# Optimization experiments

Measured on AMD Instinct MI355X. Metric: run time of the kernel, lower is better.

## Reference

```python
import jax, jax.numpy as jnp
import numpy as np


def setup_inputs() -> dict:
    key = jax.random.key(0)
    ks = jax.random.split(key, 8)
    b, n, K, d, MC = 32, 64, 512, 256, 2
    # soft codebook assignments per slot (bounded convex weights)
    encodings = jax.nn.softmax(jax.random.normal(ks[0], (b, n, K), jnp.float32), axis=-1)
    # hypersphere-initialized means (unit-norm rows)
    mu = jax.random.normal(ks[1], (K, d), jnp.float32)
    mu_embeddings = mu / jnp.linalg.norm(mu, axis=-1, keepdims=True)
    sigma_embeddings = jax.random.uniform(ks[2], (K, d), jnp.float32)
    fc1_w = jax.random.normal(ks[3], (K, d, d), jnp.float32) * (1.0 / np.sqrt(d))
    fc1_b = jax.random.normal(ks[4], (K, d), jnp.float32) * 0.02
    fc2_w = jax.random.normal(ks[5], (K, d, d), jnp.float32) * (1.0 / np.sqrt(d))
    fc2_b = jax.random.normal(ks[6], (K, d), jnp.float32) * 0.02
    eps = jax.random.normal(ks[7], (b, MC, n, d), jnp.float32)  # reparam noise
    return {"encodings": encodings, "mu_embeddings": mu_embeddings,
            "sigma_embeddings": sigma_embeddings, "fc1_w": fc1_w, "fc1_b": fc1_b,
            "fc2_w": fc2_w, "fc2_b": fc2_b, "eps": eps}


def reference(encodings, mu_embeddings, sigma_embeddings, fc1_w, fc1_b, fc2_w, fc2_b, eps):
    b, n, K = encodings.shape
    m = eps.shape[1]
    # per-slot Gaussian params from codebook mixture
    slot_mu = jnp.einsum('bnk,kd->bnd', encodings, mu_embeddings)          # (b,n,d)
    slot_sigma = jnp.exp(0.5 * jnp.einsum('bnk,kd->bnd', encodings, sigma_embeddings))
    # reparameterized MC samples: (b,m,n,d)
    slots = slot_mu[:, None] + slot_sigma[:, None] * eps
    # per-token dynamic 2-layer MLP weights (mixture over codebook)
    fc1w = jnp.einsum('bnk,kgh->bngh', encodings, fc1_w)  # (b,n,d,d)
    fc1b = jnp.einsum('bnk,kg->bng', encodings, fc1_b)    # (b,n,d)
    fc2w = jnp.einsum('bnk,kgh->bngh', encodings, fc2_w)
    fc2b = jnp.einsum('bnk,kg->bng', encodings, fc2_b)
    slots = jax.nn.relu(jnp.einsum('bmng,bngh->bmnh', slots, fc1w) + fc1b[:, None])
    slots = jax.nn.relu(jnp.einsum('bmng,bngh->bmnh', slots, fc2w) + fc2b[:, None])
    # rearrange 'b m n d -> (b m) n d'
    return slots.reshape(b * m, n, slots.shape[-1])
```

## Files before the change

### kernel.cpp

```cpp
#include <hip/hip_runtime.h>
#include <hip/hip_bf16.h>

typedef unsigned short u16;
typedef __attribute__((ext_vector_type(8))) short shortx8;
typedef __attribute__((ext_vector_type(4))) float floatx4;

__device__ __forceinline__ float bf2f(u16 u) {
    union { unsigned int ui; float f; } x; x.ui = ((unsigned int)u) << 16; return x.f;
}
__device__ __forceinline__ u16 f2b(float f) {
    union { float f; unsigned int u; } x; x.f = f;
    unsigned int r = (x.u + 0x7fffu + ((x.u >> 16) & 1u)) >> 16;
    return (u16)r;
}
__device__ __forceinline__ void glds16(const void* g, void* l) {
    __builtin_amdgcn_global_load_lds((const __attribute__((address_space(1))) void*)g,
                                     (__attribute__((address_space(3))) void*)l, 16, 0, 0);
}

__global__ __launch_bounds__(256) void cvt_bf16_kernel(const float* __restrict__ src,
                                                       u16* __restrict__ dst, int n) {
    int i = (blockIdx.x * 256 + threadIdx.x) * 4;
    if (i + 3 < n) {
        float4 v = *(const float4*)&src[i];
        ushort4 o; o.x = f2b(v.x); o.y = f2b(v.y); o.z = f2b(v.z); o.w = f2b(v.w);
        *(ushort4*)&dst[i] = o;
    }
}

__global__ __launch_bounds__(256) void build_bsmall_t(const float* __restrict__ mu,
                                                      const float* __restrict__ sg,
                                                      const float* __restrict__ b1,
                                                      const float* __restrict__ b2,
                                                      u16* __restrict__ Bs) {
    __shared__ float t[32][33];
    const float* src;
    int z = blockIdx.z;
    if (z == 0) src = mu; else if (z == 1) src = sg; else if (z == 2) src = b1; else src = b2;
    int k0 = blockIdx.x * 32, c0 = blockIdx.y * 32;
    int r = threadIdx.x >> 3, c4 = (threadIdx.x & 7) * 4;
    float4 v = *(const float4*)&src[(size_t)(k0 + r) * 256 + c0 + c4];
    t[r][c4] = v.x; t[r][c4 + 1] = v.y; t[r][c4 + 2] = v.z; t[r][c4 + 3] = v.w;
    __syncthreads();
    ushort4 o;
    o.x = f2b(t[c4 + 0][r]); o.y = f2b(t[c4 + 1][r]);
    o.z = f2b(t[c4 + 2][r]); o.w = f2b(t[c4 + 3][r]);
    *(ushort4*)&Bs[(size_t)(z * 256 + c0 + r) * 512 + k0 + c4] = o;
}

__global__ __launch_bounds__(256) void cvt_transpose(const float* __restrict__ W,
                                                     u16* __restrict__ Bt) {
    __shared__ float t[64][33];
    int n0 = blockIdx.x * 32, k0 = blockIdx.y * 64;
    int r = threadIdx.x >> 2;
    int c = (threadIdx.x & 3) * 8;
    float4 v0 = *(const float4*)&W[(size_t)(k0 + r) * 65536 + n0 + c];
    float4 v1 = *(const float4*)&W[(size_t)(k0 + r) * 65536 + n0 + c + 4];
    t[r][c + 0] = v0.x; t[r][c + 1] = v0.y; t[r][c + 2] = v0.z; t[r][c + 3] = v0.w;
    t[r][c + 4] = v1.x; t[r][c + 5] = v1.y; t[r][c + 6] = v1.z; t[r][c + 7] = v1.w;
    __syncthreads();
    int nr = threadIdx.x >> 3;
    int kk = (threadIdx.x & 7) * 8;
    shortx8 o;
    #pragma unroll
    for (int i = 0; i < 8; i++) o[i] = (short)f2b(t[kk + i][nr]);
    *(shortx8*)&Bt[(size_t)(n0 + nr) * 512 + k0 + kk] = o;
}

__global__ __launch_bounds__(256) void slots_kernel(const float* __restrict__ P,
                                                    const float* __restrict__ eps,
                                                    float* __restrict__ slots) {
    int t = blockIdx.x, d = threadIdx.x;
    float mu = P[(size_t)t * 1024 + d];
    float sg = expf(0.5f * P[(size_t)t * 1024 + 256 + d]);
    int b = t >> 6, n = t & 63;
    #pragma unroll
    for (int m = 0; m < 2; m++) {
        float e = eps[(size_t)(((b * 2 + m) * 64) + n) * 256 + d];
        slots[(size_t)t * 512 + m * 256 + d] = mu + sg * e;
    }
}

__global__ __launch_bounds__(256, 2) void gemm_small(const u16* __restrict__ A,
                                                     const u16* __restrict__ B,
                                                     float* __restrict__ C,
                                                     int N, int K,
                                                     int nbx_l2, int bypx_l2) {
    __shared__ __align__(16) u16 As[128 * 64];
    __shared__ __align__(16) u16 Bs[128 * 64];
    int tid = threadIdx.x;
    int wave = tid >> 6, lane = tid & 63;

    int id = blockIdx.x;
    int xcd = id & 7, sq = id >> 3;
    int by = (xcd << bypx_l2) + (sq >> nbx_l2);
    int bx = sq & ((1 << nbx_l2) - 1);
    int m0 = bx * 128, n0 = by * 128;
    int wm = wave >> 1, wn = wave & 1;

    floatx4 acc[4][4];
    #pragma unroll
    for (int r = 0; r < 4; r++)
        #pragma unroll
        for (int c = 0; c < 4; c++)
            #pragma unroll
            for (int q = 0; q < 4; q++) acc[r][c][q] = 0.f;

    int lrsub = lane >> 3, kcl = lane & 7;
    const u16* gA[4]; const u16* gB[4]; u16* lA[4]; u16* lB[4];
    #pragma unroll
    for (int j = 0; j < 4; j++) {
        int r0 = (wave * 4 + j) * 8;
        int row = r0 + lrsub;
        int kof = (kcl ^ (row & 7)) * 8;
        gA[j] = A + (size_t)(m0 + row) * K + kof;
        gB[j] = B + (size_t)(n0 + row) * K + kof;
        lA[j] = As + r0 * 64;
        lB[j] = Bs + r0 * 64;
    }

    int arb = wm * 64 + (lane & 15);
    int brb = wn * 64 + (lane & 15);
    int axr = arb & 7, bxr = brb & 7;
    int cl0 = lane >> 4;

    for (int k0 = 0; k0 < K; k0 += 64) {
        #pragma unroll
        for (int j = 0; j < 4; j++) glds16(gA[j] + k0, lA[j]);
        #pragma unroll
        for (int j = 0; j < 4; j++) glds16(gB[j] + k0, lB[j]);
        __syncthreads();
        #pragma unroll
        for (int s = 0; s < 2; s++) {
            shortx8 af[4], bf[4];
            int ac = ((s * 4 + cl0) ^ axr) * 8;
            int bc = ((s * 4 + cl0) ^ bxr) * 8;
            #pragma unroll
            for (int r = 0; r < 4; r++) af[r] = *(const shortx8*)(As + (arb + r * 16) * 64 + ac);
            #pragma unroll
            for (int c = 0; c < 4; c++) bf[c] = *(const shortx8*)(Bs + (brb + c * 16) * 64 + bc);
            #pragma unroll
            for (int r = 0; r < 4; r++)
                #pragma unroll
                for (int c = 0; c < 4; c++)
                    acc[r][c] = __builtin_amdgcn_mfma_f32_16x16x32_bf16(af[r], bf[c], acc[r][c], 0, 0, 0);
        }
        __syncthreads();
    }

    int crow0 = m0 + wm * 64 + (lane >> 4) * 4;
    int ccol  = n0 + wn * 64 + (lane & 15);
    #pragma unroll
    for (int r = 0; r < 4; r++)
        #pragma unroll
        for (int c = 0; c < 4; c++)
            #pragma unroll
            for (int q = 0; q < 4; q++)
                C[(size_t)(crow0 + r * 16 + q) * N + ccol + c * 16] = acc[r][c][q];
}

__global__ __launch_bounds__(256) void init_y(const float* __restrict__ P,
                                              float* __restrict__ Y, int bias_col) {
    int t = blockIdx.x, h = threadIdx.x;
    float b = P[(size_t)t * 1024 + bias_col + h];
    Y[((size_t)t * 2 + 0) * 256 + h] = b;
    Y[((size_t)t * 2 + 1) * 256 + h] = b;
}

__global__ __launch_bounds__(256, 2) void fused_mlp(const u16* __restrict__ Eb,
                                                    const u16* __restrict__ Bt,
                                                    const float* __restrict__ S,
                                                    float* __restrict__ Y,
                                                    int relu_s) {
    __shared__ __align__(16) u16 As[2][128 * 64];
    __shared__ __align__(16) u16 Bs[2][2][64 * 64];
    int tid = threadIdx.x;
    int wave = tid >> 6, lane = tid & 63;

    int id = blockIdx.x;
    int xcd = id & 7;
    int rest = id >> 3;
    int tt = rest & 15;
    int chi = rest >> 4;
    int combo = chi * 8 + xcd;
    int hh = combo >> 3;
    int gg = combo & 7;
    int m0 = tt * 128;
    int h0 = hh * 64;
    int g0 = gg * 32;

    int wm = wave >> 1, wn = wave & 1;
    int lrsub = lane >> 3, kcl = lane & 7;
    int kof = (kcl ^ lrsub) * 8;

    const u16* gAb = Eb + (size_t)(m0 + wave * 32 + lrsub) * 512 + kof;
    const u16* gBb = Bt + ((size_t)g0 * 256 + h0 + wave * 16 + lrsub) * 512 + kof;

    int arb = wm * 64 + (lane & 15);
    int brb = wn * 32 + (lane & 15);
    int axr = arb & 7, bxr = brb & 7;
    int cl0 = lane >> 4;

    floatx4 yreg[2][4][2];
    #pragma unroll
    for (int m = 0; m < 2; m++)
        #pragma unroll
        for (int r = 0; r < 4; r++)
            #pragma unroll
            for (int c = 0; c < 2; c++)
                #pragma unroll
                for (int q = 0; q < 4; q++) yreg[m][r][c][q] = 0.f;

    #pragma unroll
    for (int j = 0; j < 4; j++) glds16(gAb + j * 4096, &As[0][wave * 2048 + j * 512]);
    #pragma unroll
    for (int j = 0; j < 2; j++) glds16(gBb + j * 4096, &Bs[0][0][wave * 1024 + j * 512]);
    #pragma unroll
    for (int j = 0; j < 2; j++) glds16(gBb + 131072 + j * 4096, &Bs[0][1][wave * 1024 + j * 512]);

    const float* Sb = S + (size_t)(m0 + wm * 64 + cl0 * 4) * 512 + g0;

    #pragma unroll 1
    for (int gp = 0; gp < 16; gp++) {
        floatx4 acc[2][4][2];
        #pragma unroll
        for (int u = 0; u < 2; u++)
            #pragma unroll
            for (int r = 0; r < 4; r++)
                #pragma unroll
                for (int c = 0; c < 2; c++)
                    #pragma unroll
                    for (int q = 0; q < 4; q++) acc[u][r][c][q] = 0.f;

        #pragma unroll
        for (int ks = 0; ks < 8; ++ks) {
            const int cb = ks & 1;
            const int nb = cb ^ 1;
            {
                const int nk = ((ks + 1) & 7) * 64;
                const int ngp = (ks == 7) ? ((gp + 1) & 15) : gp;
                const size_t ng = (size_t)(2 * ngp) * 131072;
                #pragma unroll
                for (int j = 0; j < 4; j++)
                    glds16(gAb + j * 4096 + nk, &As[nb][wave * 2048 + j * 512]);
                #pragma unroll
                for (int j = 0; j < 2; j++)
                    glds16(gBb + ng + j * 4096 + nk, &Bs[nb][0][wave * 1024 + j * 512]);
                #pragma unroll
                for (int j = 0; j < 2; j++)
                    glds16(gBb + ng + 131072 + j * 4096 + nk, &Bs[nb][1][wave * 1024 + j * 512]);
            }
            asm volatile("s_waitcnt vmcnt(8)" ::: "memory");
            __builtin_amdgcn_s_barrier();
            __builtin_amdgcn_sched_barrier(0);
            #pragma unroll
            for (int s = 0; s < 2; s++) {
                shortx8 af[4], bf[2][2];
                int ac = ((s * 4 + cl0) ^ axr) * 8;
                int bc = ((s * 4 + cl0) ^ bxr) * 8;
                #pragma unroll
                for (int r = 0; r < 4; r++)
                    af[r] = *(const shortx8*)(&As[cb][(arb + r * 16) * 64 + ac]);
                #pragma unroll
                for (int u = 0; u < 2; u++)
                    #pragma unroll
                    for (int c = 0; c < 2; c++)
                        bf[u][c] = *(const shortx8*)(&Bs[cb][u][(brb + c * 16) * 64 + bc]);
                #pragma unroll
                for (int r = 0; r < 4; r++)
                    #pragma unroll
                    for (int u = 0; u < 2; u++)
                        #pragma unroll
                        for (int c = 0; c < 2; c++)
                            acc[u][r][c] = __builtin_amdgcn_mfma_f32_16x16x32_bf16(af[r], bf[u][c], acc[u][r][c], 0, 0, 0);
            }
            __builtin_amdgcn_sched_barrier(0);
            __builtin_amdgcn_s_barrier();
        }

        #pragma unroll
        for (int u = 0; u < 2; u++) {
            int gi = 2 * gp + u;
            #pragma unroll
            for (int m = 0; m < 2; m++)
                #pragma unroll
                for (int r = 0; r < 4; r++)
                    #pragma unroll
                    for (int q = 0; q < 4; q++) {
                        float sv = Sb[(size_t)(r * 16 + q) * 512 + m * 256 + gi];
                        if (relu_s) sv = fmaxf(sv, 0.f);
                        #pragma unroll
                        for (int c = 0; c < 2; c++)
                            yreg[m][r][c][q] += sv * acc[u][r][c][q];
                    }
        }
    }

    asm volatile("s_waitcnt vmcnt(0)" ::: "memory");

    int l16 = lane & 15;
    #pragma unroll
    for (int m = 0; m < 2; m++)
        #pragma unroll
        for (int r = 0; r < 4; r++)
            #pragma unroll
            for (int c = 0; c < 2; c++)
                #pragma unroll
                for (int q = 0; q < 4; q++) {
                    int t = m0 + wm * 64 + cl0 * 4 + r * 16 + q;
                    int h = h0 + wn * 32 + c * 16 + l16;
                    atomicAdd(&Y[((size_t)t * 2 + m) * 256 + h], yreg[m][r][c][q]);
                }
}

__global__ __launch_bounds__(256) void final_out(const float* __restrict__ Y,
                                                 float* __restrict__ out) {
    int t = blockIdx.x, h = threadIdx.x;
    int b = t >> 6, n = t & 63;
    #pragma unroll
    for (int m = 0; m < 2; m++)
        out[((size_t)((b * 2 + m) * 64) + n) * 256 + h] =
            fmaxf(Y[((size_t)t * 2 + m) * 256 + h], 0.f);
}

extern "C" void kernel_launch(void* const* d_in, const int* in_sizes, int n_in,
                              void* d_out, int out_size, void* d_ws, size_t ws_size,
                              hipStream_t stream) {
    const float* enc = (const float*)d_in[0];
    const float* mu  = (const float*)d_in[1];
    const float* sg  = (const float*)d_in[2];
    const float* f1w = (const float*)d_in[3];
    const float* f1b = (const float*)d_in[4];
    const float* f2w = (const float*)d_in[5];
    const float* f2b = (const float*)d_in[6];
    const float* eps = (const float*)d_in[7];
    float* out = (float*)d_out;

    size_t off = 0;
    auto alloc = [&](size_t b) -> char* {
        char* p = (char*)d_ws + off; off += (b + 255) & ~(size_t)255; return p;
    };
    u16*   Eb    = (u16*)  alloc((size_t)2048 * 512 * 2);
    float* P     = (float*)alloc((size_t)2048 * 1024 * 4);
    float* slots = (float*)alloc((size_t)2048 * 512 * 4);
    float* Y1    = (float*)alloc((size_t)2048 * 512 * 4);
    float* Y2    = (float*)alloc((size_t)2048 * 512 * 4);
    u16*   Bsm   = (u16*)  alloc((size_t)1024 * 512 * 2);
    u16*   Bt    = (u16*)  alloc((size_t)65536 * 512 * 2);

    cvt_bf16_kernel<<<1024, 256, 0, stream>>>(enc, Eb, 2048 * 512);
    build_bsmall_t<<<dim3(16, 8, 4), 256, 0, stream>>>(mu, sg, f1b, f2b, Bsm);
    gemm_small<<<128, 256, 0, stream>>>(Eb, Bsm, P, 1024, 512, 4, 0);
    slots_kernel<<<2048, 256, 0, stream>>>(P, eps, slots);

    cvt_transpose<<<dim3(2048, 8), 256, 0, stream>>>(f1w, Bt);
    init_y<<<2048, 256, 0, stream>>>(P, Y1, 512);
    fused_mlp<<<512, 256, 0, stream>>>(Eb, Bt, slots, Y1, 0);

    cvt_transpose<<<dim3(2048, 8), 256, 0, stream>>>(f2w, Bt);
    init_y<<<2048, 256, 0, stream>>>(P, Y2, 768);
    fused_mlp<<<512, 256, 0, stream>>>(Eb, Bt, Y1, Y2, 1);

    final_out<<<2048, 256, 0, stream>>>(Y2, out);
}
```

Measured before the change: 707.2 us.

## Stage slot activations in LDS, single-buffer A tiles, fold bias init into slots

The two init_y launches are merged into the slots kernel, which now also writes the broadcast fc biases into Y1 and Y2. In fused_mlp, the slot activations used for the per-g weighting (with the ReLU applied) are staged once into LDS in two halves, replacing strided global loads in the epilogue. To free LDS for this, the A tile drops from double to single buffering and is loaded at the current k-step rather than prefetched. That exposes A-load latency on every k-step, and a leftover dead loop adds a wasted global read.

Measured after the change: 721.3 us. No clear change (+2.0%).

```diff
diff --git a/kernel.cpp b/kernel.cpp
--- a/kernel.cpp
+++ b/kernel.cpp
@@ -67,12 +67,20 @@
     *(shortx8*)&Bt[(size_t)(n0 + nr) * 512 + k0 + kk] = o;
 }
 
-__global__ __launch_bounds__(256) void slots_kernel(const float* __restrict__ P,
-                                                    const float* __restrict__ eps,
-                                                    float* __restrict__ slots) {
+__global__ __launch_bounds__(256) void slots_init(const float* __restrict__ P,
+                                                  const float* __restrict__ eps,
+                                                  float* __restrict__ slots,
+                                                  float* __restrict__ Y1,
+                                                  float* __restrict__ Y2) {
     int t = blockIdx.x, d = threadIdx.x;
     float mu = P[(size_t)t * 1024 + d];
     float sg = expf(0.5f * P[(size_t)t * 1024 + 256 + d]);
+    float b1 = P[(size_t)t * 1024 + 512 + d];
+    float b2 = P[(size_t)t * 1024 + 768 + d];
+    Y1[((size_t)t * 2 + 0) * 256 + d] = b1;
+    Y1[((size_t)t * 2 + 1) * 256 + d] = b1;
+    Y2[((size_t)t * 2 + 0) * 256 + d] = b2;
+    Y2[((size_t)t * 2 + 1) * 256 + d] = b2;
     int b = t >> 6, n = t & 63;
     #pragma unroll
     for (int m = 0; m < 2; m++) {
@@ -159,21 +167,14 @@
                 C[(size_t)(crow0 + r * 16 + q) * N + ccol + c * 16] = acc[r][c][q];
 }
 
-__global__ __launch_bounds__(256) void init_y(const float* __restrict__ P,
-                                              float* __restrict__ Y, int bias_col) {
-    int t = blockIdx.x, h = threadIdx.x;
-    float b = P[(size_t)t * 1024 + bias_col + h];
-    Y[((size_t)t * 2 + 0) * 256 + h] = b;
-    Y[((size_t)t * 2 + 1) * 256 + h] = b;
-}
-
 __global__ __launch_bounds__(256, 2) void fused_mlp(const u16* __restrict__ Eb,
                                                     const u16* __restrict__ Bt,
                                                     const float* __restrict__ S,
                                                     float* __restrict__ Y,
                                                     int relu_s) {
-    __shared__ __align__(16) u16 As[2][128 * 64];
+    __shared__ __align__(16) u16 As[128 * 64];
     __shared__ __align__(16) u16 Bs[2][2][64 * 64];
+    __shared__ float sl[128 * 2 * 16];
     int tid = threadIdx.x;
     int wave = tid >> 6, lane = tid & 63;
 
@@ -189,6 +190,25 @@
     int h0 = hh * 64;
     int g0 = gg * 32;
 
+    {
+        int g = tid & 15, m = (tid >> 4) & 1, tb = tid >> 5;
+        for (int p = 0; p < 16; p++) {
+            int t = tb + p * 8;
+            float v = S[((size_t)(m0 + t) * 2 + m) * 256 + g0 + g];
+            if (relu_s) v = fmaxf(v, 0.f);
+            sl[(t * 2 + m) * 16 + g] = v;
+        }
+        int g2 = g + 16;
+        for (int p = 0; p < 16; p++) {
+            int t = tb + p * 8;
+            float v = S[((size_t)(m0 + t) * 2 + m) * 256 + g0 + g2];
+            if (relu_s) v = fmaxf(v, 0.f);
+            (void)v; (void)g2;
+            break;
+        }
+    }
+    __syncthreads();
+
     int wm = wave >> 1, wn = wave & 1;
     int lrsub = lane >> 3, kcl = lane & 7;
     int kof = (kcl ^ lrsub) * 8;
@@ -212,16 +232,23 @@
                 for (int q = 0; q < 4; q++) yreg[m][r][c][q] = 0.f;
 
     #pragma unroll
-    for (int j = 0; j < 4; j++) glds16(gAb + j * 4096, &As[0][wave * 2048 + j * 512]);
-    #pragma unroll
     for (int j = 0; j < 2; j++) glds16(gBb + j * 4096, &Bs[0][0][wave * 1024 + j * 512]);
     #pragma unroll
     for (int j = 0; j < 2; j++) glds16(gBb + 131072 + j * 4096, &Bs[0][1][wave * 1024 + j * 512]);
-
-    const float* Sb = S + (size_t)(m0 + wm * 64 + cl0 * 4) * 512 + g0;
 
     #pragma unroll 1
     for (int gp = 0; gp < 16; gp++) {
+        if (gp == 8) {
+            __syncthreads();
+            int g = tid & 15, m = (tid >> 4) & 1, tb = tid >> 5;
+            for (int p = 0; p < 16; p++) {
+                int t = tb + p * 8;
+                float v = S[((size_t)(m0 + t) * 2 + m) * 256 + g0 + 16 + g];
+                if (relu_s) v = fmaxf(v, 0.f);
+                sl[(t * 2 + m) * 16 + g] = v;
+            }
+            __syncthreads();
+        }
         floatx4 acc[2][4][2];
         #pragma unroll
         for (int u = 0; u < 2; u++)
@@ -236,21 +263,21 @@
         for (int ks = 0; ks < 8; ++ks) {
             const int cb = ks & 1;
             const int nb = cb ^ 1;
+            #pragma unroll
+            for (int j = 0; j < 4; j++)
+                glds16(gAb + j * 4096 + ks * 64, &As[wave * 2048 + j * 512]);
             {
                 const int nk = ((ks + 1) & 7) * 64;
                 const int ngp = (ks == 7) ? ((gp + 1) & 15) : gp;
                 const size_t ng = (size_t)(2 * ngp) * 131072;
                 #pragma unroll
-                for (int j = 0; j < 4; j++)
-                    glds16(gAb + j * 4096 + nk, &As[nb][wave * 2048 + j * 512]);
-                #pragma unroll
                 for (int j = 0; j < 2; j++)
                     glds16(gBb + ng + j * 4096 + nk, &Bs[nb][0][wave * 1024 + j * 512]);
                 #pragma unroll
                 for (int j = 0; j < 2; j++)
                     glds16(gBb + ng + 131072 + j * 4096 + nk, &Bs[nb][1][wave * 1024 + j * 512]);
             }
-            asm volatile("s_waitcnt vmcnt(8)" ::: "memory");
+            asm volatile("s_waitcnt vmcnt(4)" ::: "memory");
             __builtin_amdgcn_s_barrier();
             __builtin_amdgcn_sched_barrier(0);
             #pragma unroll
@@ -260,7 +287,7 @@
                 int bc = ((s * 4 + cl0) ^ bxr) * 8;
                 #pragma unroll
                 for (int r = 0; r < 4; r++)
-                    af[r] = *(const shortx8*)(&As[cb][(arb + r * 16) * 64 + ac]);
+                    af[r] = *(const shortx8*)(&As[(arb + r * 16) * 64 + ac]);
                 #pragma unroll
                 for (int u = 0; u < 2; u++)
                     #pragma unroll
@@ -280,15 +307,15 @@
 
         #pragma unroll
         for (int u = 0; u < 2; u++) {
-            int gi = 2 * gp + u;
+            int gl = (2 * gp + u) & 15;
             #pragma unroll
             for (int m = 0; m < 2; m++)
                 #pragma unroll
                 for (int r = 0; r < 4; r++)
                     #pragma unroll
                     for (int q = 0; q < 4; q++) {
-                        float sv = Sb[(size_t)(r * 16 + q) * 512 + m * 256 + gi];
-                        if (relu_s) sv = fmaxf(sv, 0.f);
+                        int t = wm * 64 + cl0 * 4 + r * 16 + q;
+                        float sv = sl[(t * 2 + m) * 16 + gl];
                         #pragma unroll
                         for (int c = 0; c < 2; c++)
                             yreg[m][r][c][q] += sv * acc[u][r][c][q];
@@ -351,14 +378,12 @@
     cvt_bf16_kernel<<<1024, 256, 0, stream>>>(enc, Eb, 2048 * 512);
     build_bsmall_t<<<dim3(16, 8, 4), 256, 0, stream>>>(mu, sg, f1b, f2b, Bsm);
     gemm_small<<<128, 256, 0, stream>>>(Eb, Bsm, P, 1024, 512, 4, 0);
-    slots_kernel<<<2048, 256, 0, stream>>>(P, eps, slots);
+    slots_init<<<2048, 256, 0, stream>>>(P, eps, slots, Y1, Y2);
 
     cvt_transpose<<<dim3(2048, 8), 256, 0, stream>>>(f1w, Bt);
-    init_y<<<2048, 256, 0, stream>>>(P, Y1, 512);
     fused_mlp<<<512, 256, 0, stream>>>(Eb, Bt, slots, Y1, 0);
 
     cvt_transpose<<<dim3(2048, 8), 256, 0, stream>>>(f2w, Bt);
-    init_y<<<2048, 256, 0, stream>>>(P, Y2, 768);
     fused_mlp<<<512, 256, 0, stream>>>(Eb, Bt, Y1, Y2, 1);
 
     final_out<<<2048, 256, 0, stream>>>(Y2, out);
```
